# Kernel optimization log

Hardware: AMD Instinct MI355X
Metric: run time of the kernel (lower is better)

## Reference

```python
import jax, jax.numpy as jnp
import numpy as np

# N nodes, E edges; lmax=6 -> L=(lmax+1)^2=49; lmax_reduce=(lmax+1)//2=3 -> LR=16
# (matches hardcoded c[:, :16, :] in the torch source); M=25 is the basis size of the
# lmax=4 'middle' irreps in cg_interaction2; NY = num_y_rotations.
# node_interaction's reshape(b, basis_num, c) forces sphere_channels_reduce == hidden_channels.
N, E, L, LR, M, NY, C, H, NB = 2048, 4096, 49, 16, 25, 3, 128, 128, 128
INV_SQRT_3 = float(1.0 / np.sqrt(3.0))


def _silu(v):
    return v * jax.nn.sigmoid(v)


def setup_inputs():
    key = jax.random.key(0)
    ks = jax.random.split(key, 24)
    rn = lambda k, s, sc=1.0: (sc * jax.random.normal(k, s)).astype(jnp.float32)
    return {
        "x": rn(ks[0], (N, L, C)),
        "x_time": rn(ks[1], (1, 1)),        # forward sets x_time = None; unused
        "x_glovec": rn(ks[2], (N, LR)),
        "x_edge": rn(ks[3], (E, NB)),
        "edge_index": jax.random.randint(ks[4], (2, E), 0, N),
        "edge_vec": rn(ks[5], (E, 3)),      # unused by forward body
        "node_sh_inv": rn(ks[6], (1,)),     # unused by forward body
        "node_self": rn(ks[7], (1,)),       # unused by forward body
        # dense bilinear stand-ins for the e3nn FullyConnectedTensorProducts
        "W_cg1": rn(ks[8], (L, L, M), 0.05),
        "W_cg21": rn(ks[9], (L, M, L), 0.05),
        "W_cg22": rn(ks[10], (L, M, L), 0.05),
        # node_interaction1 MLP
        "Wn1a": rn(ks[11], (LR * (C + 1), H), (LR * (C + 1)) ** -0.5),
        "bn1a": jnp.zeros((H,), jnp.float32),
        "Wn1b": rn(ks[12], (H, LR * C), H ** -0.5),
        "bn1b": jnp.zeros((LR * C,), jnp.float32),
        # node_interaction2 MLP
        "Wn2a": rn(ks[13], (LR * (C + 1), H), (LR * (C + 1)) ** -0.5),
        "bn2a": jnp.zeros((H,), jnp.float32),
        "Wn2b": rn(ks[14], (H, LR * C), H ** -0.5),
        "bn2b": jnp.zeros((LR * C,), jnp.float32),
        # fc1_dist / fc1_edge_proj / fc2_edge
        "Wd": rn(ks[15], (NB, H), NB ** -0.5),
        "bd": jnp.zeros((H,), jnp.float32),
        "Wp1": rn(ks[16], (LR * C, H), (LR * C) ** -0.5),
        "bp1": jnp.zeros((H,), jnp.float32),
        "Wp2": rn(ks[17], (H, LR * C), H ** -0.5),
        "bp2": jnp.zeros((LR * C,), jnp.float32),
        # per-edge Wigner-style rotation buffers (geometry-derived in the original)
        "wigner": rn(ks[18], (E, NY, LR, L), L ** -0.5),      # Rotate: full -> reduced, NY taps
        "wigner_inv": rn(ks[19], (E, L, LR), LR ** -0.5),     # RotateInv: reduced -> full
        "wig_node": rn(ks[20], (E, LR, LR), LR ** -0.5),      # Rotate_edge / Rotate_edgeInv
    }


def _forward(x, x_glovec, x_edge, W_cg1, W_cg21, W_cg22, Wn1a, bn1a, Wn1b, bn1b,
             Wn2a, bn2a, Wn2b, bn2b, Wd, bd, Wp1, bp1, Wp2, bp2,
             wigner, wigner_inv, wig_node, edge_index):
    src, dst = edge_index[0], edge_index[1]
    xe = _silu(x_edge @ Wd + bd)                              # [E,H]  fc1_dist
    xs, xt = x[src], x[dst]                                   # [E,L,C] edge gathers
    gs, gt = x_glovec[src], x_glovec[dst]                     # [E,LR]

    # cg_interaction2: mean over channels, CG bilinears, broadcast residual
    xm, ym = xs.mean(2), xt.mean(2)                           # [E,L]
    mid = jnp.einsum('ei,ej,ijo->eo', xm, ym, W_cg1)          # [E,M]  cg1
    sh_cg = xs + xt \
        + jnp.einsum('ei,ej,ijo->eo', xm, mid, W_cg21)[..., None] \
        + jnp.einsum('ei,ej,ijo->eo', ym, mid, W_cg22)[..., None]  # [E,L,C]

    def node_int(ne, ndf, Wa, ba, Wb, bb):
        # Rotate_edgeInv (transpose of per-edge rotation) on reduced basis
        ne = jnp.einsum('eji,ejc->eic', wig_node, ne[:, :LR, :])       # [E,LR,C]
        feat = jnp.concatenate([ne, (ne.mean(2) * ndf)[..., None]], axis=2)
        h = _silu(feat.reshape(E, LR * (C + 1)) @ Wa + ba)             # node_fc1
        h = _silu(h @ Wb + bb).reshape(E, LR, C)                       # node_fc3
        return jnp.einsum('eij,ejc->eic', wig_node, h)                 # Rotate_edge

    sh = node_int(xs, gt, Wn1a, bn1a, Wn1b, bn1b) \
       + node_int(xt, gs, Wn2a, bn2a, Wn2b, bn2b)                      # [E,LR,C]
    c = sh_cg.at[:, :LR, :].add(sh)

    def rotate(z):  # sphharm.Rotate: [E,L,C] -> [E*NY, LR*C]
        return jnp.einsum('enrb,ebc->enrc', wigner, z).reshape(E * NY, LR * C)

    msg = rotate(xs) + rotate(xt) + rotate(c)
    m = _silu(msg @ Wp1 + bp1)                                # [E*NY,H] fc1_edge_proj
    m = (m.reshape(E, NY, H) * xe[:, None, :]).reshape(E * NY, H)
    m = _silu(m @ Wp2 + bp2)                                  # fc2_edge
    m = m.reshape(E, NY, LR, C).mean(1)                       # CombineYRotations
    out = jnp.einsum('ebr,erc->ebc', wigner_inv, m) * INV_SQRT_3  # RotateInv
    return out                                                # [E,L,C]


def reference(x, x_time, x_glovec, x_edge, edge_index, edge_vec, node_sh_inv,
              node_self, W_cg1, W_cg21, W_cg22, Wn1a, bn1a, Wn1b, bn1b,
              Wn2a, bn2a, Wn2b, bn2b, Wd, bd, Wp1, bp1, Wp2, bp2,
              wigner, wigner_inv, wig_node):
    # x_time / edge_vec / node_sh_inv / node_self are unused (x_time = None in source)
    return _forward(x, x_glovec, x_edge, W_cg1, W_cg21, W_cg22, Wn1a, bn1a, Wn1b,
                    bn1b, Wn2a, bn2a, Wn2b, bn2b, Wd, bd, Wp1, bp1, Wp2, bp2,
                    wigner, wigner_inv, wig_node, edge_index)
```

## Files before the change

kernel.cpp:

```cpp
#include <hip/hip_runtime.h>
#include <hip/hip_bf16.h>

typedef __hip_bfloat16 bf16;
typedef __attribute__((ext_vector_type(8))) short short8;
typedef __attribute__((ext_vector_type(4))) float f32x4;

#define NN 2048
#define EE 4096
#define LL 49
#define LRR 16
#define NYY 3
#define CC 128
#define HH 128

#define K1P 2432
#define K2P 2496

__device__ __forceinline__ float siluf(float v) { return v * (1.0f / (1.0f + __expf(-v))); }
__device__ __forceinline__ bf16 f2b(float v) { return __float2bfloat16(v); }

struct TJob { const float* in; bf16* out; int K, N, Kp; };
struct TJobs { TJob j[6]; };

__global__ __launch_bounds__(256) void transpose_cvt_kernel(TJobs jobs) {
  TJob jb = jobs.j[blockIdx.y];
  int i = blockIdx.x * 256 + threadIdx.x;
  if (i < jb.N * jb.Kp) {
    int n = i / jb.Kp, k = i - n * jb.Kp;
    jb.out[i] = (k < jb.K) ? f2b(jb.in[(long)k * jb.N + n]) : f2b(0.f);
  }
}

__global__ __launch_bounds__(256) void cg_prep_kernel(
    const float* __restrict__ Wcg1, const float* __restrict__ Wcg21,
    const float* __restrict__ Wcg22, bf16* __restrict__ BT1, bf16* __restrict__ BT2) {
  int i = blockIdx.x * 256 + threadIdx.x;
  if (blockIdx.y == 0) {
    if (i < 32 * K1P) {
      int o = i / K1P, k = i - o * K1P;
      float v = (o < 25 && k < 2401) ? Wcg1[k * 25 + o] : 0.f;
      BT1[i] = f2b(v);
    }
  } else {
    if (i < 64 * K2P) {
      int o = i / K2P, k = i - o * K2P;
      float v = 0.f;
      if (o < 49) {
        if (k < 1225) v = Wcg21[k * 49 + o];
        else if (k < 2450) v = Wcg22[(k - 1225) * 49 + o];
      }
      BT2[i] = f2b(v);
    }
  }
}

__global__ __launch_bounds__(256) void node_mean_kernel(const float* __restrict__ x,
                                                        float* __restrict__ xmean) {
  int row = blockIdx.x * 4 + (threadIdx.x >> 6);
  int lane = threadIdx.x & 63;
  const float* p = x + (long)row * CC;
  float s = p[lane] + p[lane + 64];
  for (int off = 32; off > 0; off >>= 1) s += __shfl_down(s, off);
  if (lane == 0) xmean[row] = s * (1.0f / 128.0f);
}

__global__ __launch_bounds__(256) void build_p1_kernel(
    const float* __restrict__ xmean, const int* __restrict__ eidx, bf16* __restrict__ P1) {
  __shared__ float sxm[49], sym[49];
  int e = blockIdx.x, tid = threadIdx.x;
  int s = eidx[e], d = eidx[EE + e];
  if (tid < 49) { sxm[tid] = xmean[s * 49 + tid]; sym[tid] = xmean[d * 49 + tid]; }
  __syncthreads();
  for (int idx = tid; idx < K1P; idx += 256) {
    float v = 0.f;
    if (idx < 2401) { int i = idx / 49, j = idx - i * 49; v = sxm[i] * sym[j]; }
    P1[(long)e * K1P + idx] = f2b(v);
  }
}

__global__ __launch_bounds__(256) void build_p2_kernel(
    const float* __restrict__ xmean, const float* __restrict__ mid,
    const int* __restrict__ eidx, bf16* __restrict__ P2) {
  __shared__ float sxm[49], sym[49], smid[25];
  int e = blockIdx.x, tid = threadIdx.x;
  int s = eidx[e], d = eidx[EE + e];
  if (tid < 49) { sxm[tid] = xmean[s * 49 + tid]; sym[tid] = xmean[d * 49 + tid]; }
  if (tid >= 64 && tid < 89) smid[tid - 64] = mid[e * 32 + tid - 64];
  __syncthreads();
  for (int idx = tid; idx < K2P; idx += 256) {
    float v = 0.f;
    if (idx < 1225) { int i = idx / 25, m = idx - i * 25; v = sxm[i] * smid[m]; }
    else if (idx < 2450) { int kk = idx - 1225; int i = kk / 25, m = kk - i * 25; v = sym[i] * smid[m]; }
    P2[(long)e * K2P + idx] = f2b(v);
  }
}

template <int NI>
__global__ __launch_bounds__(256) void gemm_smalln(
    const bf16* __restrict__ A, const bf16* __restrict__ BT,
    float* __restrict__ C, int K) {
  __shared__ short As[64 * 64];
  __shared__ short Bs[NI * 16 * 64];
  const int tid = threadIdx.x, w = tid >> 6, lane = tid & 63;
  const int lm = lane & 15, q = lane >> 4;
  const int bm = blockIdx.x * 64;
  f32x4 acc[NI];
#pragma unroll
  for (int ni = 0; ni < NI; ++ni) acc[ni] = (f32x4){0.f, 0.f, 0.f, 0.f};
  for (int k0 = 0; k0 < K; k0 += 64) {
    __syncthreads();
#pragma unroll
    for (int it = 0; it < 2; ++it) {
      int lc = it * 256 + tid;
      int m = lc >> 3, k8 = lc & 7;
      uint4 v = *(const uint4*)((const char*)A + ((long)(bm + m) * K + k0 + k8 * 8) * 2);
      *(uint4*)&As[(m * 8 + (k8 ^ (m & 7))) * 8] = v;
    }
#pragma unroll
    for (int it = 0; it < NI / 2; ++it) {
      int lc = it * 256 + tid;
      int n = lc >> 3, k8 = lc & 7;
      uint4 v = *(const uint4*)((const char*)BT + ((long)n * K + k0 + k8 * 8) * 2);
      *(uint4*)&Bs[(n * 8 + (k8 ^ (n & 7))) * 8] = v;
    }
    __syncthreads();
#pragma unroll
    for (int ks = 0; ks < 2; ++ks) {
      short8 af = *(const short8*)&As[(w * 16 + lm) * 64 + ((ks * 4 + q) ^ (lm & 7)) * 8];
#pragma unroll
      for (int ni = 0; ni < NI; ++ni) {
        short8 bfr = *(const short8*)&Bs[(ni * 16 + lm) * 64 + ((ks * 4 + q) ^ (lm & 7)) * 8];
        acc[ni] = __builtin_amdgcn_mfma_f32_16x16x32_bf16(af, bfr, acc[ni], 0, 0, 0);
      }
    }
  }
#pragma unroll
  for (int ni = 0; ni < NI; ++ni) {
    int col = ni * 16 + lm;
#pragma unroll
    for (int r = 0; r < 4; ++r) {
      int row = bm + w * 16 + q * 4 + r;
      C[(long)row * (NI * 16) + col] = acc[ni][r];
    }
  }
}

__global__ __launch_bounds__(256) void build_feat_kernel(
    const float* __restrict__ x, const float* __restrict__ x_glovec,
    const float* __restrict__ wig_node, const int* __restrict__ eidx,
    bf16* __restrict__ featst) {
  __shared__ float wig[256];
  __shared__ float xa[2048], xb[2048], tmp[2048];
  int e = blockIdx.x, tid = threadIdx.x;
  int s = eidx[e], d = eidx[EE + e];
  wig[tid] = wig_node[e * 256 + tid];
  if (tid < 48) {
    featst[(long)e * 2112 + 2064 + tid] = f2b(0.f);
    featst[(long)(EE + e) * 2112 + 2064 + tid] = f2b(0.f);
  }
  for (int idx = tid; idx < 2048; idx += 256) {
    int l = idx >> 7, c = idx & 127;
    xa[idx] = x[((long)s * LL + l) * CC + c];
    xb[idx] = x[((long)d * LL + l) * CC + c];
  }
  __syncthreads();
  for (int idx = tid; idx < 2048; idx += 256) {
    int i = idx >> 7, c = idx & 127;
    float a = 0.f;
#pragma unroll
    for (int j = 0; j < 16; ++j) a += wig[j * 16 + i] * xa[j * 128 + c];
    tmp[idx] = a;
    featst[(long)e * 2112 + i * 129 + c] = f2b(a);
  }
  __syncthreads();
  if (tid < 16) {
    float m = 0.f;
    for (int c = 0; c < 128; ++c) m += tmp[tid * 128 + c];
    featst[(long)e * 2112 + tid * 129 + 128] = f2b(m * (1.0f / 128.0f) * x_glovec[(long)d * 16 + tid]);
  }
  __syncthreads();
  for (int idx = tid; idx < 2048; idx += 256) {
    int i = idx >> 7, c = idx & 127;
    float a = 0.f;
#pragma unroll
    for (int j = 0; j < 16; ++j) a += wig[j * 16 + i] * xb[j * 128 + c];
    tmp[idx] = a;
    featst[(long)(EE + e) * 2112 + i * 129 + c] = f2b(a);
  }
  __syncthreads();
  if (tid < 16) {
    float m = 0.f;
    for (int c = 0; c < 128; ++c) m += tmp[tid * 128 + c];
    featst[(long)(EE + e) * 2112 + tid * 129 + 128] = f2b(m * (1.0f / 128.0f) * x_glovec[(long)s * 16 + tid]);
  }
}

__global__ __launch_bounds__(256) void gemm_f32_silu(
    const float* __restrict__ A, const float* __restrict__ B,
    const float* __restrict__ bias, float* __restrict__ C, int M, int N, int K) {
  __shared__ float As[16][68];
  __shared__ float Bs[16][64];
  const int tid = threadIdx.x;
  const int bm = blockIdx.x * 64, bn = blockIdx.y * 64;
  const int tx = tid & 15, ty = tid >> 4;
  const int ar = tid >> 2, ak = (tid & 3) * 4;
  const int br = tid >> 4, bc = (tid & 15) * 4;
  float acc[4][4] = {};
  const float* Ap = A + (long)(bm + ar) * K + ak;
  const float* Bp = B + (long)br * N + bn + bc;
  for (int k0 = 0; k0 < K; k0 += 16) {
    const float4 av = *(const float4*)(Ap + k0);
    const float4 bv = *(const float4*)(Bp + (long)k0 * N);
    __syncthreads();
    As[ak + 0][ar] = av.x; As[ak + 1][ar] = av.y;
    As[ak + 2][ar] = av.z; As[ak + 3][ar] = av.w;
    *(float4*)&Bs[br][bc] = bv;
    __syncthreads();
#pragma unroll
    for (int k = 0; k < 16; ++k) {
      const float4 a = *(const float4*)&As[k][ty * 4];
      const float4 b = *(const float4*)&Bs[k][tx * 4];
      acc[0][0] += a.x * b.x; acc[0][1] += a.x * b.y; acc[0][2] += a.x * b.z; acc[0][3] += a.x * b.w;
      acc[1][0] += a.y * b.x; acc[1][1] += a.y * b.y; acc[1][2] += a.y * b.z; acc[1][3] += a.y * b.w;
      acc[2][0] += a.z * b.x; acc[2][1] += a.z * b.y; acc[2][2] += a.z * b.z; acc[2][3] += a.z * b.w;
      acc[3][0] += a.w * b.x; acc[3][1] += a.w * b.y; acc[3][2] += a.w * b.z; acc[3][3] += a.w * b.w;
    }
  }
#pragma unroll
  for (int i = 0; i < 4; ++i) {
    int row = bm + ty * 4 + i;
#pragma unroll
    for (int j = 0; j < 4; ++j) {
      int col = bn + tx * 4 + j;
      C[(long)row * N + col] = siluf(acc[i][j] + bias[col]);
    }
  }
}

template <int BM, bool SILU, bool XE, bool OUT_BF16>
__global__ __launch_bounds__(256) void gemm_mfma(
    const bf16* __restrict__ A, const bf16* __restrict__ B0, const bf16* __restrict__ B1,
    const float* __restrict__ bias0, const float* __restrict__ bias1,
    const float* __restrict__ xe, void* __restrict__ Cout,
    int M, int N, int K, int half) {
  constexpr int MI = BM / 32;
  __shared__ short As[BM * 64];
  __shared__ short Bs[128 * 64];
  const int tid = threadIdx.x;
  const int w = tid >> 6, lane = tid & 63;
  const int lm = lane & 15, q = lane >> 4;
  const int bm = blockIdx.x * BM, bn = blockIdx.y * 128;
  const int wm = (w & 1) * (BM / 2), wn = (w >> 1) * 64;
  const bf16* Bp = (bm < half) ? B0 : B1;
  const float* bias = (bm < half) ? bias0 : bias1;

  f32x4 acc[MI][4];
#pragma unroll
  for (int mi = 0; mi < MI; ++mi)
#pragma unroll
    for (int ni = 0; ni < 4; ++ni) acc[mi][ni] = (f32x4){0.f, 0.f, 0.f, 0.f};

  for (int k0 = 0; k0 < K; k0 += 64) {
    __syncthreads();
#pragma unroll
    for (int it = 0; it < BM / 32; ++it) {
      int lc = it * 256 + tid;
      int m = lc >> 3, k8 = lc & 7;
      uint4 v = *(const uint4*)((const char*)A + ((long)(bm + m) * K + k0 + k8 * 8) * 2);
      *(uint4*)&As[(m * 8 + (k8 ^ (m & 7))) * 8] = v;
    }
#pragma unroll
    for (int it = 0; it < 4; ++it) {
      int lc = it * 256 + tid;
      int n = lc >> 3, k8 = lc & 7;
      uint4 v = *(const uint4*)((const char*)Bp + ((long)(bn + n) * K + k0 + k8 * 8) * 2);
      *(uint4*)&Bs[(n * 8 + (k8 ^ (n & 7))) * 8] = v;
    }
    __syncthreads();
#pragma unroll
    for (int ks = 0; ks < 2; ++ks) {
      short8 af[MI], bfr[4];
#pragma unroll
      for (int mi = 0; mi < MI; ++mi) {
        int row = wm + mi * 16 + lm;
        af[mi] = *(const short8*)&As[row * 64 + ((ks * 4 + q) ^ (lm & 7)) * 8];
      }
#pragma unroll
      for (int ni = 0; ni < 4; ++ni) {
        int row = wn + ni * 16 + lm;
        bfr[ni] = *(const short8*)&Bs[row * 64 + ((ks * 4 + q) ^ (lm & 7)) * 8];
      }
#pragma unroll
      for (int mi = 0; mi < MI; ++mi)
#pragma unroll
        for (int ni = 0; ni < 4; ++ni)
          acc[mi][ni] = __builtin_amdgcn_mfma_f32_16x16x32_bf16(af[mi], bfr[ni], acc[mi][ni], 0, 0, 0);
    }
  }
#pragma unroll
  for (int mi = 0; mi < MI; ++mi) {
#pragma unroll
    for (int ni = 0; ni < 4; ++ni) {
      int col = bn + wn + ni * 16 + lm;
      float bcol = bias[col];
#pragma unroll
      for (int r = 0; r < 4; ++r) {
        int row = bm + wm + mi * 16 + q * 4 + r;
        float v = acc[mi][ni][r] + bcol;
        if (SILU) v = siluf(v);
        if (XE) v *= xe[(row / 3) * HH + col];
        if (OUT_BF16) ((bf16*)Cout)[(long)row * N + col] = f2b(v);
        else ((float*)Cout)[(long)row * N + col] = v;
      }
    }
  }
}

__global__ __launch_bounds__(512, 4) void rotate_msg_fused_kernel(
    const float* __restrict__ x, const float* __restrict__ wigner,
    const int* __restrict__ eidx, const float* __restrict__ asum,
    const float* __restrict__ o1, const float* __restrict__ o2,
    const float* __restrict__ wig_node, bf16* __restrict__ msg) {
  __shared__ bf16 Ah[48 * 64], Al[48 * 64];
  __shared__ bf16 zTh[128 * 64], zTl[128 * 64];
  __shared__ float z[49 * 132];
  __shared__ float osum[16 * 128];
  __shared__ float wig[256];
  __shared__ float as_s[49];
  const int e = blockIdx.x, tid = threadIdx.x;
  const int s = eidx[e], d = eidx[EE + e];
  const int w = tid >> 6, lane = tid & 63;
  const int lm = lane & 15, q = lane >> 4;

  if (tid < 49) as_s[tid] = asum[e * 64 + tid];
  if (tid >= 64 && tid < 128) {
    int i = tid - 64;
    *(float4*)&wig[i * 4] = *(const float4*)&wig_node[(long)e * 256 + i * 4];
  }
  {
    float4 a = *(const float4*)&o1[(long)e * 2048 + tid * 4];
    float4 b = *(const float4*)&o2[(long)e * 2048 + tid * 4];
    float4 v; v.x = a.x + b.x; v.y = a.y + b.y; v.z = a.z + b.z; v.w = a.w + b.w;
    *(float4*)&osum[tid * 4] = v;
  }
  for (int i = tid; i < 48 * 15; i += 512) {
    int m = i / 15, k = 49 + (i - m * 15);
    int off = m * 64 + (((k >> 3) ^ (m & 7)) << 3) + (k & 7);
    Ah[off] = f2b(0.f); Al[off] = f2b(0.f);
  }
  for (int i4 = tid; i4 < 588; i4 += 512) {
    float4 v4 = *(const float4*)&wigner[(long)e * 2352 + i4 * 4];
    int i = i4 * 4;
    int m = i / 49, k = i - m * 49;
    float vv[4] = {v4.x, v4.y, v4.z, v4.w};
#pragma unroll
    for (int j = 0; j < 4; ++j) {
      bf16 h = f2b(vv[j]);
      bf16 l = f2b(vv[j] - __bfloat162float(h));
      int off = m * 64 + (((k >> 3) ^ (m & 7)) << 3) + (k & 7);
      Ah[off] = h; Al[off] = l;
      if (++k == 49) { k = 0; ++m; }
    }
  }
  __syncthreads();

  {
    const float* xs = x + (long)s * (LL * CC);
    const float* xt = x + (long)d * (LL * CC);
    for (int i4 = tid; i4 < 49 * 32; i4 += 512) {
      int l = i4 >> 5, c4 = i4 & 31;
      float4 a = *(const float4*)&xs[l * 128 + c4 * 4];
      float4 b = *(const float4*)&xt[l * 128 + c4 * 4];
      float ad = as_s[l];
      float4 v;
      v.x = 2.f * (a.x + b.x) + ad;
      v.y = 2.f * (a.y + b.y) + ad;
      v.z = 2.f * (a.z + b.z) + ad;
      v.w = 2.f * (a.w + b.w) + ad;
      if (l < 16) {
#pragma unroll
        for (int j = 0; j < 16; ++j) {
          float wv = wig[l * 16 + j];
          float4 o = *(const float4*)&osum[j * 128 + c4 * 4];
          v.x += wv * o.x; v.y += wv * o.y; v.z += wv * o.z; v.w += wv * o.w;
        }
      }
      *(float4*)&z[l * 132 + c4 * 4] = v;
    }
  }
  __syncthreads();

  {
    int b = lane;
#pragma unroll
    for (int i = 0; i < 16; ++i) {
      int c = w * 16 + i;
      float v = (b < 49) ? z[b * 132 + c] : 0.f;
      bf16 h = f2b(v);
      bf16 l = f2b(v - __bfloat162float(h));
      int off = c * 64 + (((b >> 3) ^ (c & 7)) << 3) + (b & 7);
      zTh[off] = h; zTl[off] = l;
    }
  }
  __syncthreads();

  short8 ah[3][2], alo[3][2], bh[2], bl[2];
#pragma unroll
  for (int mi = 0; mi < 3; ++mi)
#pragma unroll
    for (int ks = 0; ks < 2; ++ks) {
      int off = (mi * 16 + lm) * 64 + (((ks * 4 + q) ^ (lm & 7)) << 3);
      ah[mi][ks] = *(const short8*)&Ah[off];
      alo[mi][ks] = *(const short8*)&Al[off];
    }
#pragma unroll
  for (int ks = 0; ks < 2; ++ks) {
    int off = (w * 16 + lm) * 64 + (((ks * 4 + q) ^ (lm & 7)) << 3);
    bh[ks] = *(const short8*)&zTh[off];
    bl[ks] = *(const short8*)&zTl[off];
  }
  f32x4 acc[3];
#pragma unroll
  for (int mi = 0; mi < 3; ++mi) acc[mi] = (f32x4){0.f, 0.f, 0.f, 0.f};
#pragma unroll
  for (int mi = 0; mi < 3; ++mi)
#pragma unroll
    for (int ks = 0; ks < 2; ++ks) {
      acc[mi] = __builtin_amdgcn_mfma_f32_16x16x32_bf16(ah[mi][ks], bh[ks], acc[mi], 0, 0, 0);
      acc[mi] = __builtin_amdgcn_mfma_f32_16x16x32_bf16(ah[mi][ks], bl[ks], acc[mi], 0, 0, 0);
      acc[mi] = __builtin_amdgcn_mfma_f32_16x16x32_bf16(alo[mi][ks], bh[ks], acc[mi], 0, 0, 0);
    }
  {
    int c = w * 16 + lm;
#pragma unroll
    for (int mi = 0; mi < 3; ++mi) {
      long base = ((long)e * 3 + mi) * 2048 + c;
#pragma unroll
      for (int r = 0; r < 4; ++r)
        msg[base + (q * 4 + r) * 128] = f2b(acc[mi][r]);
    }
  }
}

__global__ __launch_bounds__(256) void out_kernel(
    const float* __restrict__ m2, const float* __restrict__ wigner_inv,
    float* __restrict__ out) {
  __shared__ float mr[2048];
  __shared__ float wv[784];
  int e = blockIdx.x, tid = threadIdx.x;
  for (int idx = tid; idx < 2048; idx += 256)
    mr[idx] = (m2[((long)e * 3 + 0) * 2048 + idx] + m2[((long)e * 3 + 1) * 2048 + idx] +
               m2[((long)e * 3 + 2) * 2048 + idx]) * (1.0f / 3.0f);
  for (int idx = tid; idx < 784; idx += 256) wv[idx] = wigner_inv[(long)e * 784 + idx];
  __syncthreads();
  for (int idx = tid; idx < 6272; idx += 256) {
    int bq = idx >> 7, c = idx & 127;
    const float* wp = wv + bq * 16;
    float a = 0.f;
#pragma unroll
    for (int r = 0; r < 16; ++r) a += wp[r] * mr[r * 128 + c];
    out[(long)e * 6272 + idx] = a * 0.57735026918962576f;
  }
}

extern "C" void kernel_launch(void* const* d_in, const int* in_sizes, int n_in,
                              void* d_out, int out_size, void* d_ws, size_t ws_size,
                              hipStream_t stream) {
  (void)in_sizes; (void)n_in; (void)out_size; (void)ws_size;
  const float* x        = (const float*)d_in[0];
  const float* x_glovec = (const float*)d_in[2];
  const float* x_edge   = (const float*)d_in[3];
  const int*   eidx     = (const int*)d_in[4];
  const float* W_cg1   = (const float*)d_in[8];
  const float* W_cg21  = (const float*)d_in[9];
  const float* W_cg22  = (const float*)d_in[10];
  const float* Wn1a = (const float*)d_in[11];
  const float* bn1a = (const float*)d_in[12];
  const float* Wn1b = (const float*)d_in[13];
  const float* bn1b = (const float*)d_in[14];
  const float* Wn2a = (const float*)d_in[15];
  const float* bn2a = (const float*)d_in[16];
  const float* Wn2b = (const float*)d_in[17];
  const float* bn2b = (const float*)d_in[18];
  const float* Wd   = (const float*)d_in[19];
  const float* bd   = (const float*)d_in[20];
  const float* Wp1  = (const float*)d_in[21];
  const float* bp1  = (const float*)d_in[22];
  const float* Wp2  = (const float*)d_in[23];
  const float* bp2  = (const float*)d_in[24];
  const float* wigner     = (const float*)d_in[25];
  const float* wigner_inv = (const float*)d_in[26];
  const float* wig_node   = (const float*)d_in[27];

  char* W = (char*)d_ws;
  bf16*  featst = (bf16*)(W + 0);
  float* ostack = (float*)(W + 34603008);
  float* m2     = (float*)(W + 0);
  bf16*  msg    = (bf16*)(W + 135266304);
  bf16*  P1     = (bf16*)(W + 135266304);
  bf16*  P2     = (bf16*)(W + 155189248);
  bf16*  hstack = (bf16*)(W + 185597952);
  bf16*  m1     = (bf16*)(W + 187695104);
  float* p_xe   = (float*)(W + 190840832);
  float* p_xmean= (float*)(W + 192937984);
  bf16*  BTa    = (bf16*)(W + 194142208);
  bf16*  BTb    = (bf16*)(W + 195223552);
  bf16*  BTp1   = (bf16*)(W + 196272128);
  bf16*  BTp2   = (bf16*)(W + 196796416);
  float* p_asum = (float*)(W + 197320704);
  float* p_mid  = (float*)(W + 198369280);
  bf16*  BT1    = (bf16*)(W + 198893568);
  bf16*  BT2    = (bf16*)(W + 199049216);

  TJobs tj;
  tj.j[0] = {Wn1a, BTa,            2064, 128, 2112};
  tj.j[1] = {Wn2a, BTa + 270336,   2064, 128, 2112};
  tj.j[2] = {Wn1b, BTb,            128, 2048, 128};
  tj.j[3] = {Wn2b, BTb + 262144,   128, 2048, 128};
  tj.j[4] = {Wp1,  BTp1,           2048, 128, 2048};
  tj.j[5] = {Wp2,  BTp2,           128, 2048, 128};
  transpose_cvt_kernel<<<dim3(1056, 6), 256, 0, stream>>>(tj);
  cg_prep_kernel<<<dim3(624, 2), 256, 0, stream>>>(W_cg1, W_cg21, W_cg22, BT1, BT2);

  node_mean_kernel<<<(NN * LL) / 4, 256, 0, stream>>>(x, p_xmean);
  build_p1_kernel<<<EE, 256, 0, stream>>>(p_xmean, eidx, P1);
  gemm_smalln<2><<<EE / 64, 256, 0, stream>>>(P1, BT1, p_mid, K1P);
  build_p2_kernel<<<EE, 256, 0, stream>>>(p_xmean, p_mid, eidx, P2);
  gemm_smalln<4><<<EE / 64, 256, 0, stream>>>(P2, BT2, p_asum, K2P);

  gemm_f32_silu<<<dim3(EE / 64, 2), 256, 0, stream>>>(x_edge, Wd, bd, p_xe, EE, HH, 128);
  build_feat_kernel<<<EE, 256, 0, stream>>>(x, x_glovec, wig_node, eidx, featst);
  gemm_mfma<64, true, false, true><<<dim3(128, 1), 256, 0, stream>>>(
      featst, BTa, BTa + 270336, bn1a, bn2a, nullptr, hstack, 8192, 128, 2112, 4096);
  gemm_mfma<128, true, false, false><<<dim3(64, 16), 256, 0, stream>>>(
      hstack, BTb, BTb + 262144, bn1b, bn2b, nullptr, ostack, 8192, 2048, 128, 4096);
  rotate_msg_fused_kernel<<<EE, 512, 0, stream>>>(
      x, wigner, eidx, p_asum, ostack, ostack + (long)4096 * 2048, wig_node, msg);
  gemm_mfma<64, true, true, true><<<dim3(192, 1), 256, 0, stream>>>(
      msg, BTp1, BTp1, bp1, bp1, p_xe, m1, 12288, 128, 2048, 1 << 30);
  gemm_mfma<128, true, false, false><<<dim3(96, 16), 256, 0, stream>>>(
      m1, BTp2, BTp2, bp2, bp2, nullptr, m2, 12288, 2048, 128, 1 << 30);
  out_kernel<<<EE, 256, 0, stream>>>(m2, wigner_inv, (float*)d_out);
}
```

Measured before the change: 576.5 us.

## Fuse node MLP second layers with sum, and fc2_edge with Y-combine and inverse rotation

```diff
diff --git a/kernel.cpp b/kernel.cpp
--- a/kernel.cpp
+++ b/kernel.cpp
@@ -18,6 +18,9 @@
 
 __device__ __forceinline__ float siluf(float v) { return v * (1.0f / (1.0f + __expf(-v))); }
 __device__ __forceinline__ bf16 f2b(float v) { return __float2bfloat16(v); }
+__device__ __forceinline__ float getc(float4 v, int i) {
+  return i == 0 ? v.x : i == 1 ? v.y : i == 2 ? v.z : v.w;
+}
 
 struct TJob { const float* in; bf16* out; int K, N, Kp; };
 struct TJobs { TJob j[6]; };
@@ -316,15 +319,99 @@
   }
 }
 
+__global__ __launch_bounds__(256) void gemm_osum(
+    const bf16* __restrict__ A, const bf16* __restrict__ B0w, const bf16* __restrict__ B1w,
+    const float* __restrict__ bias0, const float* __restrict__ bias1,
+    float* __restrict__ osum) {
+  __shared__ short As[128 * 64];
+  __shared__ short Bs[128 * 64];
+  const int tid = threadIdx.x;
+  const int w = tid >> 6, lane = tid & 63;
+  const int lm = lane & 15, q = lane >> 4;
+  const int bm = blockIdx.x * 128, bn = blockIdx.y * 128;
+  const int wm = (w & 1) * 64, wn = (w >> 1) * 64;
+  f32x4 ov[4][4];
+  f32x4 acc[4][4];
+#pragma unroll
+  for (int mi = 0; mi < 4; ++mi)
+#pragma unroll
+    for (int ni = 0; ni < 4; ++ni) acc[mi][ni] = (f32x4){0.f, 0.f, 0.f, 0.f};
+
+#pragma unroll 1
+  for (int src = 0; src < 2; ++src) {
+    const bf16* Ap = A + (long)src * 4096 * 128;
+    const bf16* Bp = src ? B1w : B0w;
+#pragma unroll 1
+    for (int k0 = 0; k0 < 128; k0 += 64) {
+      __syncthreads();
+#pragma unroll
+      for (int it = 0; it < 4; ++it) {
+        int lc = it * 256 + tid;
+        int m = lc >> 3, k8 = lc & 7;
+        uint4 v = *(const uint4*)((const char*)Ap + ((long)(bm + m) * 128 + k0 + k8 * 8) * 2);
+        *(uint4*)&As[(m * 8 + (k8 ^ (m & 7))) * 8] = v;
+      }
+#pragma unroll
+      for (int it = 0; it < 4; ++it) {
+        int lc = it * 256 + tid;
+        int n = lc >> 3, k8 = lc & 7;
+        uint4 v = *(const uint4*)((const char*)Bp + ((long)(bn + n) * 128 + k0 + k8 * 8) * 2);
+        *(uint4*)&Bs[(n * 8 + (k8 ^ (n & 7))) * 8] = v;
+      }
+      __syncthreads();
+#pragma unroll
+      for (int ks = 0; ks < 2; ++ks) {
+        short8 af[4], bfr[4];
+#pragma unroll
+        for (int mi = 0; mi < 4; ++mi)
+          af[mi] = *(const short8*)&As[(wm + mi * 16 + lm) * 64 + ((ks * 4 + q) ^ (lm & 7)) * 8];
+#pragma unroll
+        for (int ni = 0; ni < 4; ++ni)
+          bfr[ni] = *(const short8*)&Bs[(wn + ni * 16 + lm) * 64 + ((ks * 4 + q) ^ (lm & 7)) * 8];
+#pragma unroll
+        for (int mi = 0; mi < 4; ++mi)
+#pragma unroll
+          for (int ni = 0; ni < 4; ++ni)
+            acc[mi][ni] = __builtin_amdgcn_mfma_f32_16x16x32_bf16(af[mi], bfr[ni], acc[mi][ni], 0, 0, 0);
+      }
+    }
+    if (src == 0) {
+#pragma unroll
+      for (int mi = 0; mi < 4; ++mi)
+#pragma unroll
+        for (int ni = 0; ni < 4; ++ni) {
+          int col = bn + wn + ni * 16 + lm;
+          float bc = bias0[col];
+#pragma unroll
+          for (int r = 0; r < 4; ++r) ov[mi][ni][r] = siluf(acc[mi][ni][r] + bc);
+#pragma unroll
+          for (int r = 0; r < 4; ++r) acc[mi][ni][r] = 0.f;
+        }
+    }
+  }
+#pragma unroll
+  for (int mi = 0; mi < 4; ++mi)
+#pragma unroll
+    for (int ni = 0; ni < 4; ++ni) {
+      int col = bn + wn + ni * 16 + lm;
+      float bc = bias1[col];
+#pragma unroll
+      for (int r = 0; r < 4; ++r) {
+        int row = bm + wm + mi * 16 + q * 4 + r;
+        osum[(long)row * 2048 + col] = ov[mi][ni][r] + siluf(acc[mi][ni][r] + bc);
+      }
+    }
+}
+
 __global__ __launch_bounds__(512, 4) void rotate_msg_fused_kernel(
     const float* __restrict__ x, const float* __restrict__ wigner,
     const int* __restrict__ eidx, const float* __restrict__ asum,
-    const float* __restrict__ o1, const float* __restrict__ o2,
-    const float* __restrict__ wig_node, bf16* __restrict__ msg) {
+    const float* __restrict__ osum, const float* __restrict__ wig_node,
+    bf16* __restrict__ msg) {
   __shared__ bf16 Ah[48 * 64], Al[48 * 64];
   __shared__ bf16 zTh[128 * 64], zTl[128 * 64];
   __shared__ float z[49 * 132];
-  __shared__ float osum[16 * 128];
+  __shared__ float osum_s[16 * 128];
   __shared__ float wig[256];
   __shared__ float as_s[49];
   const int e = blockIdx.x, tid = threadIdx.x;
@@ -337,12 +424,7 @@
     int i = tid - 64;
     *(float4*)&wig[i * 4] = *(const float4*)&wig_node[(long)e * 256 + i * 4];
   }
-  {
-    float4 a = *(const float4*)&o1[(long)e * 2048 + tid * 4];
-    float4 b = *(const float4*)&o2[(long)e * 2048 + tid * 4];
-    float4 v; v.x = a.x + b.x; v.y = a.y + b.y; v.z = a.z + b.z; v.w = a.w + b.w;
-    *(float4*)&osum[tid * 4] = v;
-  }
+  *(float4*)&osum_s[tid * 4] = *(const float4*)&osum[(long)e * 2048 + tid * 4];
   for (int i = tid; i < 48 * 15; i += 512) {
     int m = i / 15, k = 49 + (i - m * 15);
     int off = m * 64 + (((k >> 3) ^ (m & 7)) << 3) + (k & 7);
@@ -381,7 +463,7 @@
 #pragma unroll
         for (int j = 0; j < 16; ++j) {
           float wv = wig[l * 16 + j];
-          float4 o = *(const float4*)&osum[j * 128 + c4 * 4];
+          float4 o = *(const float4*)&osum_s[j * 128 + c4 * 4];
           v.x += wv * o.x; v.y += wv * o.y; v.z += wv * o.z; v.w += wv * o.w;
         }
       }
@@ -391,15 +473,27 @@
   __syncthreads();
 
   {
-    int b = lane;
-#pragma unroll
-    for (int i = 0; i < 16; ++i) {
-      int c = w * 16 + i;
-      float v = (b < 49) ? z[b * 132 + c] : 0.f;
-      bf16 h = f2b(v);
-      bf16 l = f2b(v - __bfloat162float(h));
-      int off = c * 64 + (((b >> 3) ^ (c & 7)) << 3) + (b & 7);
-      zTh[off] = h; zTl[off] = l;
+    const int b0 = (tid & 15) * 4;
+    const int c0 = (tid >> 4) * 4;
+    float4 rv[4];
+#pragma unroll
+    for (int j = 0; j < 4; ++j)
+      rv[j] = (b0 + j < 49) ? *(const float4*)&z[(b0 + j) * 132 + c0]
+                            : (float4){0.f, 0.f, 0.f, 0.f};
+#pragma unroll
+    for (int i = 0; i < 4; ++i) {
+      int c = c0 + i;
+      union { bf16 b[4]; unsigned long long u; } hu, lu;
+#pragma unroll
+      for (int j = 0; j < 4; ++j) {
+        float v = getc(rv[j], i);
+        bf16 h = f2b(v);
+        hu.b[j] = h;
+        lu.b[j] = f2b(v - __bfloat162float(h));
+      }
+      int off = c * 64 + (((b0 >> 3) ^ (c & 7)) << 3) + (b0 & 7);
+      *(unsigned long long*)&zTh[off] = hu.u;
+      *(unsigned long long*)&zTl[off] = lu.u;
     }
   }
   __syncthreads();
@@ -442,24 +536,87 @@
   }
 }
 
-__global__ __launch_bounds__(256) void out_kernel(
-    const float* __restrict__ m2, const float* __restrict__ wigner_inv,
+__global__ __launch_bounds__(512) void m2out_kernel(
+    const bf16* __restrict__ m1, const bf16* __restrict__ BTp2,
+    const float* __restrict__ bp2, const float* __restrict__ wigner_inv,
     float* __restrict__ out) {
-  __shared__ float mr[2048];
-  __shared__ float wv[784];
-  int e = blockIdx.x, tid = threadIdx.x;
-  for (int idx = tid; idx < 2048; idx += 256)
-    mr[idx] = (m2[((long)e * 3 + 0) * 2048 + idx] + m2[((long)e * 3 + 1) * 2048 + idx] +
-               m2[((long)e * 3 + 2) * 2048 + idx]) * (1.0f / 3.0f);
-  for (int idx = tid; idx < 784; idx += 256) wv[idx] = wigner_inv[(long)e * 784 + idx];
-  __syncthreads();
-  for (int idx = tid; idx < 6272; idx += 256) {
-    int bq = idx >> 7, c = idx & 127;
-    const float* wp = wv + bq * 16;
-    float a = 0.f;
-#pragma unroll
-    for (int r = 0; r < 16; ++r) a += wp[r] * mr[r * 128 + c];
-    out[(long)e * 6272 + idx] = a * 0.57735026918962576f;
+  __shared__ __align__(16) char sm[4096 + 32768 + 8448 + 32768];
+  short (*As)[1024] = (short(*)[1024])sm;
+  short (*Bs)[8192] = (short(*)[8192])(sm + 4096);
+  float* pbuf = (float*)(sm + 4096 + 32768);
+  float* mr   = (float*)(sm + 4096 + 32768 + 8448);
+  float* wv_s = (float*)(sm + 4096);
+
+  const int tid = threadIdx.x;
+  const int w = tid >> 6, lane = tid & 63;
+  const int lm = lane & 15, q = lane >> 4;
+  const int e0 = blockIdx.x * 4;
+
+  if (tid < 256) {
+    int n = tid >> 4, k8 = tid & 15;
+    uint4 v = (uint4){0, 0, 0, 0};
+    if (n < 12) v = *(const uint4*)((const char*)m1 + ((long)(e0 * 3 + n) * 128 + k8 * 8) * 2);
+    *(uint4*)&As[k8 >> 3][(n * 8 + ((k8 & 7) ^ (n & 7))) * 8] = v;
+  }
+
+#pragma unroll 1
+  for (int nc = 0; nc < 16; ++nc) {
+    __syncthreads();
+#pragma unroll
+    for (int it = 0; it < 4; ++it) {
+      int lc = it * 512 + tid;
+      int n = lc >> 4, k8 = lc & 15;
+      uint4 v = *(const uint4*)((const char*)BTp2 + ((long)(nc * 128 + n) * 128 + k8 * 8) * 2);
+      *(uint4*)&Bs[k8 >> 3][(n * 8 + ((k8 & 7) ^ (n & 7))) * 8] = v;
+    }
+    __syncthreads();
+    f32x4 acc = (f32x4){0.f, 0.f, 0.f, 0.f};
+#pragma unroll
+    for (int ks = 0; ks < 4; ++ks) {
+      int kh = ks >> 1, ksl = ks & 1;
+      short8 af = *(const short8*)&As[kh][(lm * 8 + ((ksl * 4 + q) ^ (lm & 7))) * 8];
+      int brow = w * 16 + lm;
+      short8 bfr = *(const short8*)&Bs[kh][(brow * 8 + ((ksl * 4 + q) ^ (brow & 7))) * 8];
+      acc = __builtin_amdgcn_mfma_f32_16x16x32_bf16(af, bfr, acc, 0, 0, 0);
+    }
+    {
+      int col = w * 16 + lm;
+      float bc = bp2[nc * 128 + col];
+#pragma unroll
+      for (int r = 0; r < 4; ++r)
+        pbuf[(q * 4 + r) * 132 + col] = siluf(acc[r] + bc);
+    }
+    __syncthreads();
+    {
+      int c = tid & 127, e4 = tid >> 7;
+      mr[e4 * 2048 + nc * 128 + c] =
+          (pbuf[(3 * e4 + 0) * 132 + c] + pbuf[(3 * e4 + 1) * 132 + c] +
+           pbuf[(3 * e4 + 2) * 132 + c]) * (1.f / 3.f);
+    }
+  }
+  __syncthreads();
+  for (int i4 = tid; i4 < 784; i4 += 512)
+    *(float4*)&wv_s[i4 * 4] = *(const float4*)&wigner_inv[(long)e0 * 784 + i4 * 4];
+  __syncthreads();
+  {
+    const int c4 = tid & 31, sb = (tid >> 5) & 3, ep = tid >> 7;
+#pragma unroll 1
+    for (int bb = 0; bb < 13; ++bb) {
+      int b = bb * 4 + sb;
+      if (b < 49) {
+        float a0 = 0.f, a1 = 0.f, a2 = 0.f, a3 = 0.f;
+#pragma unroll
+        for (int r = 0; r < 16; ++r) {
+          float wvv = wv_s[ep * 784 + b * 16 + r];
+          const float4 m = *(const float4*)&mr[ep * 2048 + r * 128 + c4 * 4];
+          a0 += wvv * m.x; a1 += wvv * m.y; a2 += wvv * m.z; a3 += wvv * m.w;
+        }
+        float4 o;
+        o.x = a0 * 0.57735026918962576f; o.y = a1 * 0.57735026918962576f;
+        o.z = a2 * 0.57735026918962576f; o.w = a3 * 0.57735026918962576f;
+        *(float4*)&out[(long)(e0 + ep) * 6272 + b * 128 + c4 * 4] = o;
+      }
+    }
   }
 }
 
@@ -494,8 +651,7 @@
 
   char* W = (char*)d_ws;
   bf16*  featst = (bf16*)(W + 0);
-  float* ostack = (float*)(W + 34603008);
-  float* m2     = (float*)(W + 0);
+  float* p_osum = (float*)(W + 34603008);
   bf16*  msg    = (bf16*)(W + 135266304);
   bf16*  P1     = (bf16*)(W + 135266304);
   bf16*  P2     = (bf16*)(W + 155189248);
@@ -532,13 +688,10 @@
   build_feat_kernel<<<EE, 256, 0, stream>>>(x, x_glovec, wig_node, eidx, featst);
   gemm_mfma<64, true, false, true><<<dim3(128, 1), 256, 0, stream>>>(
       featst, BTa, BTa + 270336, bn1a, bn2a, nullptr, hstack, 8192, 128, 2112, 4096);
-  gemm_mfma<128, true, false, false><<<dim3(64, 16), 256, 0, stream>>>(
-      hstack, BTb, BTb + 262144, bn1b, bn2b, nullptr, ostack, 8192, 2048, 128, 4096);
+  gemm_osum<<<dim3(32, 16), 256, 0, stream>>>(hstack, BTb, BTb + 262144, bn1b, bn2b, p_osum);
   rotate_msg_fused_kernel<<<EE, 512, 0, stream>>>(
-      x, wigner, eidx, p_asum, ostack, ostack + (long)4096 * 2048, wig_node, msg);
+      x, wigner, eidx, p_asum, p_osum, wig_node, msg);
   gemm_mfma<64, true, true, true><<<dim3(192, 1), 256, 0, stream>>>(
       msg, BTp1, BTp1, bp1, bp1, p_xe, m1, 12288, 128, 2048, 1 << 30);
-  gemm_mfma<128, true, false, false><<<dim3(96, 16), 256, 0, stream>>>(
-      m1, BTp2, BTp2, bp2, bp2, nullptr, m2, 12288, 2048, 128, 1 << 30);
-  out_kernel<<<EE, 256, 0, stream>>>(m2, wigner_inv, (float*)d_out);
-}
+  m2out_kernel<<<EE / 4, 512, 0, stream>>>(m1, BTp2, bp2, wigner_inv, (float*)d_out);
+}
```

New measurement: 569.6 us. About the same (-1.2%).
